# Optimization experiments

Measured on AMD Instinct MI355X. Metric: run time of the kernel, lower is better.

Reference implementation:

```python
import jax, jax.numpy as jnp
import numpy as np

N_NODES = 50000
N_EDGES = 1600000
IN_FEATS = 256
OUT_FEATS = 128
NEG_SLOPE = 0.2


def setup_inputs() -> dict:
    key = jax.random.key(0)
    k1, k2, k3, k4, k5, k6 = jax.random.split(key, 6)
    gain = np.sqrt(2.0)  # calculate_gain('relu')
    w_std = gain * np.sqrt(2.0 / (IN_FEATS + OUT_FEATS))  # xavier normal
    a_std = gain * np.sqrt(2.0 / (1 + OUT_FEATS))
    return {
        "feat": jax.random.normal(k1, (N_NODES, IN_FEATS), dtype=jnp.float32),
        "W": jax.random.normal(k2, (OUT_FEATS, IN_FEATS), dtype=jnp.float32) * w_std,
        "attn_l": jax.random.normal(k3, (1, OUT_FEATS), dtype=jnp.float32) * a_std,
        "attn_r": jax.random.normal(k4, (1, OUT_FEATS), dtype=jnp.float32) * a_std,
        "src": jax.random.randint(k5, (N_EDGES,), 0, N_NODES, dtype=jnp.int32),
        "dst": jax.random.randint(k6, (N_EDGES,), 0, N_NODES, dtype=jnp.int32),
    }


def reference(feat, W, attn_l, attn_r, src, dst):
    # h = fc(feat): [N, D]
    h = jnp.einsum("ni,di->nd", feat, W)
    # per-node attention logits
    el = jnp.sum(h * attn_l, axis=-1)  # [N]
    er = jnp.sum(h * attn_r, axis=-1)  # [N]
    # apply_edge: e_uv = el[u] + er[v], then leaky relu
    e = jax.nn.leaky_relu(el[src] + er[dst], NEG_SLOPE)  # [E]
    # edge softmax over incoming edges of each destination node
    m = jax.ops.segment_max(e, dst, num_segments=N_NODES)  # [N]
    m = jnp.where(jnp.isneginf(m), 0.0, m)  # nodes with no in-edges
    ex = jnp.exp(e - m[dst])  # [E]
    denom = jax.ops.segment_sum(ex, dst, num_segments=N_NODES)  # [N]
    alpha = ex / jnp.maximum(denom[dst], 1e-9)  # [E]
    # gspmv: rst[v] = sum_{(u->v)} alpha_uv * h[u]
    rst = jax.ops.segment_sum(h[src] * alpha[:, None], dst, num_segments=N_NODES)
    return rst
```

## Files before the change

kernel.cpp:

```cpp
#include <hip/hip_runtime.h>
#include <hip/hip_bf16.h>


#define IN_FEATS 256
#define OUT_FEATS 128
#define NBINS 256
#define CAPB_LOG 14
#define CAPB (1 << CAPB_LOG)
#define SCAT_BLOCKS 512
#define BIN_STRIDE 16

typedef __bf16 bf16x8 __attribute__((ext_vector_type(8)));
typedef float f32x4 __attribute__((ext_vector_type(4)));

__global__ void prep(const float* __restrict__ W, __bf16* __restrict__ Wb, int nw,
                     int* __restrict__ cur) {
    int i = blockIdx.x * 256 + threadIdx.x;
    if (i < nw) Wb[i] = (__bf16)W[i];
    if (i < NBINS) cur[i * BIN_STRIDE] = i << CAPB_LOG;
}

__global__ __launch_bounds__(256) void gemm_scatter(
    const float* __restrict__ feat, const __bf16* __restrict__ Wb,
    const float* __restrict__ attn_l, const float* __restrict__ attn_r,
    __bf16* __restrict__ hb, float* __restrict__ el, float* __restrict__ er,
    const int* __restrict__ src, const int* __restrict__ dst,
    int* __restrict__ bin_cur, unsigned* __restrict__ arena,
    int n, int E, int S) {
    __shared__ int h[NBINS];
    __shared__ int base[NBINS];

    if (blockIdx.x < S) {
        const int blk = blockIdx.x;
        const int t = threadIdx.x;
        h[t] = 0;
        __syncthreads();
        const int chunk = (E + SCAT_BLOCKS - 1) / SCAT_BLOCKS;
        const int beg = blk * chunk;
        const int end = min(beg + chunk, E);
        for (int i = beg + t; i < end; i += 256)
            atomicAdd(&h[dst[i] >> 8], 1);
        __syncthreads();
        if (h[t] > 0)
            base[t] = atomicAdd(&bin_cur[t * BIN_STRIDE], h[t]);
        h[t] = 0;
        __syncthreads();
        for (int i = beg + t; i < end; i += 256) {
            int d = dst[i];
            int bin = d >> 8;
            int pos = base[bin] + atomicAdd(&h[bin], 1);
            pos = min(pos, ((bin + 1) << CAPB_LOG) - 1);
            arena[pos] = ((unsigned)d << 16) | (unsigned)src[i];
        }
        return;
    }

    const int wid = threadIdx.x >> 6;
    const int lane = threadIdx.x & 63;
    const int s = lane & 15;
    const int q = lane >> 4;
    const int m0 = (blockIdx.x - S) * 64 + wid * 16;
    if (m0 >= n) return;

    const int mrow = min(m0 + s, n - 1);
    const float* arow = feat + (size_t)mrow * IN_FEATS + q * 8;

    f32x4 acc[8];
#pragma unroll
    for (int nt = 0; nt < 8; nt++) acc[nt] = (f32x4){0.f, 0.f, 0.f, 0.f};

#pragma unroll
    for (int ks = 0; ks < 8; ks++) {
        const int k0 = ks * 32;
        float4 f0 = *(const float4*)(arow + k0);
        float4 f1 = *(const float4*)(arow + k0 + 4);
        bf16x8 a;
        a[0] = (__bf16)f0.x; a[1] = (__bf16)f0.y; a[2] = (__bf16)f0.z; a[3] = (__bf16)f0.w;
        a[4] = (__bf16)f1.x; a[5] = (__bf16)f1.y; a[6] = (__bf16)f1.z; a[7] = (__bf16)f1.w;
#pragma unroll
        for (int nt = 0; nt < 8; nt++) {
            bf16x8 b = *(const bf16x8*)(Wb + (size_t)(nt * 16 + s) * IN_FEATS + k0 + q * 8);
            acc[nt] = __builtin_amdgcn_mfma_f32_16x16x32_bf16(a, b, acc[nt], 0, 0, 0);
        }
    }

    float al[8], ar[8];
#pragma unroll
    for (int nt = 0; nt < 8; nt++) {
        al[nt] = attn_l[nt * 16 + s];
        ar[nt] = attn_r[nt * 16 + s];
    }

#pragma unroll
    for (int r = 0; r < 4; r++) {
        const int row = m0 + q * 4 + r;
        const bool ok = row < n;
        float pl = 0.f, pr = 0.f;
#pragma unroll
        for (int nt = 0; nt < 8; nt++) {
            float v = acc[nt][r];
            if (ok) hb[(size_t)row * OUT_FEATS + nt * 16 + s] = (__bf16)v;
            pl += v * al[nt];
            pr += v * ar[nt];
        }
#pragma unroll
        for (int m = 1; m < 16; m <<= 1) {
            pl += __shfl_xor(pl, m);
            pr += __shfl_xor(pr, m);
        }
        if (ok && s == 0) {
            el[row] = pl;
            er[row] = pr;
        }
    }
}

__global__ __launch_bounds__(512) void build_csr(const unsigned* __restrict__ arena,
                                                 const int* __restrict__ bin_cur,
                                                 const float* __restrict__ el,
                                                 const float* __restrict__ er,
                                                 unsigned* __restrict__ edges,
                                                 int* __restrict__ row_beg,
                                                 int* __restrict__ row_end,
                                                 int N, int edges_cap) {
    __shared__ unsigned lds[CAPB];
    __shared__ int cnt[256];
    __shared__ int off[256];
    const int b = blockIdx.x;
    const int t = threadIdx.x;
    const int abeg = b << CAPB_LOG;
    const int cnt_in = min(bin_cur[b * BIN_STRIDE] - abeg, CAPB);

    for (int i = t; i < cnt_in; i += 512) lds[i] = arena[abeg + i];
    if (t < 256) cnt[t] = 0;
    __syncthreads();

    for (int i = t; i < cnt_in; i += 512)
        atomicAdd(&cnt[(lds[i] >> 16) & 255], 1);
    __syncthreads();
    if (t < 256) off[t] = cnt[t];
    __syncthreads();
    for (int o = 1; o < 256; o <<= 1) {
        int v = (t < 256 && t >= o) ? off[t - o] : 0;
        __syncthreads();
        if (t < 256) off[t] += v;
        __syncthreads();
    }
    int mycnt = 0, excl = 0;
    if (t < 256) {
        mycnt = cnt[t];
        excl = off[t] - mycnt;
    }
    __syncthreads();
    if (t < 256) {
        off[t] = excl;
        int v = (b << 8) + t;
        if (v < N) {
            row_beg[v] = abeg + excl;
            row_end[v] = abeg + excl + mycnt;
        }
        cnt[t] = 0;
    }
    __syncthreads();

    for (int i = t; i < cnt_in; i += 512) {
        unsigned e = lds[i];
        int d8 = (e >> 16) & 255;
        int u = (int)(e & 0xFFFFu);
        float x = el[u] + er[(b << 8) + d8];
        x = (x > 0.f) ? x : 0.2f * x;
        float w = __expf(x);
        int r = atomicAdd(&cnt[d8], 1);
        int pos = abeg + off[d8] + r;
        pos = min(pos, edges_cap - 1);
        edges[pos] = (__float_as_uint(w) & 0xFFFF0000u) | (unsigned)u;
    }
}

__global__ __launch_bounds__(256) void gat_kernel(const __bf16* __restrict__ hb,
                                                  const unsigned* __restrict__ edges,
                                                  const int* __restrict__ row_beg,
                                                  const int* __restrict__ row_end,
                                                  float* __restrict__ out, int n) {
    const int v = blockIdx.x * 4 + (threadIdx.x >> 6);
    if (v >= n) return;
    const int lane = threadIdx.x & 63;
    const int beg = row_beg[v];
    const int end = row_end[v];
    const unsigned* hbu = (const unsigned*)hb;

    float acc0 = 0.f, acc1 = 0.f, wsum = 0.f;
    for (int c0 = beg; c0 < end; c0 += 64) {
        const int nn = min(64, end - c0);
        int my = (c0 + lane < end) ? (int)edges[c0 + lane] : 0;

        int k = 0;
        for (; k + 8 <= nn; k += 8) {
#pragma unroll
            for (int tt = 0; tt < 8; tt++) {
                unsigned e = (unsigned)__shfl(my, k + tt);
                int u = (int)(e & 0xFFFFu);
                float w = __uint_as_float(e & 0xFFFF0000u);
                wsum += w;
                unsigned pair = hbu[(size_t)u * (OUT_FEATS / 2) + lane];
                acc0 += w * __uint_as_float(pair << 16);
                acc1 += w * __uint_as_float(pair & 0xffff0000u);
            }
        }
        for (; k < nn; k++) {
            unsigned e = (unsigned)__shfl(my, k);
            int u = (int)(e & 0xFFFFu);
            float w = __uint_as_float(e & 0xFFFF0000u);
            wsum += w;
            unsigned pair = hbu[(size_t)u * (OUT_FEATS / 2) + lane];
            acc0 += w * __uint_as_float(pair << 16);
            acc1 += w * __uint_as_float(pair & 0xffff0000u);
        }
    }
    const float dnm = fmaxf(wsum, 1e-9f);
    float2 o = make_float2(acc0 / dnm, acc1 / dnm);
    *(float2*)(out + (size_t)v * OUT_FEATS + lane * 2) = o;
}

extern "C" void kernel_launch(void* const* d_in, const int* in_sizes, int n_in,
                              void* d_out, int out_size, void* d_ws, size_t ws_size,
                              hipStream_t stream) {
    const float* feat   = (const float*)d_in[0];
    const float* W      = (const float*)d_in[1];
    const float* attn_l = (const float*)d_in[2];
    const float* attn_r = (const float*)d_in[3];
    const int*   src    = (const int*)d_in[4];
    const int*   dst    = (const int*)d_in[5];
    const int N = in_sizes[0] / IN_FEATS;
    const int E = in_sizes[4];
    float* out = (float*)d_out;

    char* p = (char*)d_ws;
    auto alloc = [&](size_t bytes) -> char* {
        char* r = p;
        p += (bytes + 255) & ~(size_t)255;
        return r;
    };
    const int nbuckets = (N + 255) / 256;
    const int edges_cap = nbuckets * CAPB;

    __bf16* hb    = (__bf16*)alloc((size_t)N * OUT_FEATS * sizeof(__bf16));
    __bf16* Wb    = (__bf16*)alloc((size_t)OUT_FEATS * IN_FEATS * sizeof(__bf16));
    float* el     = (float*)alloc((size_t)N * sizeof(float));
    float* er     = (float*)alloc((size_t)N * sizeof(float));
    int*   bin_cur = (int*)alloc((size_t)NBINS * BIN_STRIDE * sizeof(int));
    int*   row_beg = (int*)alloc((size_t)N * sizeof(int));
    int*   row_end = (int*)alloc((size_t)N * sizeof(int));
    unsigned* arena = (unsigned*)alloc((size_t)NBINS * CAPB * sizeof(unsigned));
    unsigned* edges = (unsigned*)alloc((size_t)edges_cap * sizeof(unsigned));

    prep<<<dim3((OUT_FEATS * IN_FEATS + 255) / 256), dim3(256), 0, stream>>>(
        W, Wb, OUT_FEATS * IN_FEATS, bin_cur);

    const int G = (N + 63) / 64;
    gemm_scatter<<<dim3(SCAT_BLOCKS + G), dim3(256), 0, stream>>>(
        feat, Wb, attn_l, attn_r, hb, el, er, src, dst, bin_cur, arena, N, E,
        SCAT_BLOCKS);

    build_csr<<<dim3(nbuckets), dim3(512), 0, stream>>>(arena, bin_cur, el, er, edges,
                                                        row_beg, row_end, N, edges_cap);

    gat_kernel<<<dim3((N + 3) / 4), dim3(256), 0, stream>>>(hb, edges, row_beg,
                                                            row_end, out, N);
}
```

Measured before the change: 219.6 us.

## Split scatter from GEMM and locally sort edges in LDS before global writes

Edge binning moves out of the fused GEMM kernel into its own kernel. That kernel counting-sorts each chunk of edges by bin in shared memory, so the writes to the global arena come out contiguous per bin instead of scattered. build_csr now reads the arena straight from global memory and stages the finished CSR records in LDS, then writes them out coalesced. The cost is an extra kernel launch and the loss of overlap between the GEMM and scatter work. The edges write no longer has a capacity clamp.

Result: slower. 226.2 us (+3.0%).

```diff
diff --git a/kernel.cpp b/kernel.cpp
--- a/kernel.cpp
+++ b/kernel.cpp
@@ -7,7 +7,7 @@
 #define NBINS 256
 #define CAPB_LOG 14
 #define CAPB (1 << CAPB_LOG)
-#define SCAT_BLOCKS 512
+#define SORT_CAP 4096
 #define BIN_STRIDE 16
 
 typedef __bf16 bf16x8 __attribute__((ext_vector_type(8)));
@@ -20,46 +20,16 @@
     if (i < NBINS) cur[i * BIN_STRIDE] = i << CAPB_LOG;
 }
 
-__global__ __launch_bounds__(256) void gemm_scatter(
+__global__ __launch_bounds__(256) void gemm(
     const float* __restrict__ feat, const __bf16* __restrict__ Wb,
     const float* __restrict__ attn_l, const float* __restrict__ attn_r,
     __bf16* __restrict__ hb, float* __restrict__ el, float* __restrict__ er,
-    const int* __restrict__ src, const int* __restrict__ dst,
-    int* __restrict__ bin_cur, unsigned* __restrict__ arena,
-    int n, int E, int S) {
-    __shared__ int h[NBINS];
-    __shared__ int base[NBINS];
-
-    if (blockIdx.x < S) {
-        const int blk = blockIdx.x;
-        const int t = threadIdx.x;
-        h[t] = 0;
-        __syncthreads();
-        const int chunk = (E + SCAT_BLOCKS - 1) / SCAT_BLOCKS;
-        const int beg = blk * chunk;
-        const int end = min(beg + chunk, E);
-        for (int i = beg + t; i < end; i += 256)
-            atomicAdd(&h[dst[i] >> 8], 1);
-        __syncthreads();
-        if (h[t] > 0)
-            base[t] = atomicAdd(&bin_cur[t * BIN_STRIDE], h[t]);
-        h[t] = 0;
-        __syncthreads();
-        for (int i = beg + t; i < end; i += 256) {
-            int d = dst[i];
-            int bin = d >> 8;
-            int pos = base[bin] + atomicAdd(&h[bin], 1);
-            pos = min(pos, ((bin + 1) << CAPB_LOG) - 1);
-            arena[pos] = ((unsigned)d << 16) | (unsigned)src[i];
-        }
-        return;
-    }
-
+    int n) {
     const int wid = threadIdx.x >> 6;
     const int lane = threadIdx.x & 63;
     const int s = lane & 15;
     const int q = lane >> 4;
-    const int m0 = (blockIdx.x - S) * 64 + wid * 16;
+    const int m0 = blockIdx.x * 64 + wid * 16;
     if (m0 >= n) return;
 
     const int mrow = min(m0 + s, n - 1);
@@ -115,6 +85,59 @@
     }
 }
 
+__global__ __launch_bounds__(256) void scatter(
+    const int* __restrict__ src, const int* __restrict__ dst,
+    int* __restrict__ bin_cur, unsigned* __restrict__ arena, int E, int nblk) {
+    __shared__ unsigned sorted[SORT_CAP];
+    __shared__ int h[NBINS];
+    __shared__ int off[NBINS];
+    __shared__ int gbase[NBINS];
+    const int t = threadIdx.x;
+    const int chunk = (E + nblk - 1) / nblk;
+    const int beg = blockIdx.x * chunk;
+    const int end = min(beg + chunk, E);
+
+    h[t] = 0;
+    __syncthreads();
+    for (int i = beg + t; i < end; i += 256)
+        atomicAdd(&h[dst[i] >> 8], 1);
+    __syncthreads();
+
+    off[t] = h[t];
+    __syncthreads();
+    for (int o = 1; o < 256; o <<= 1) {
+        int v = (t >= o) ? off[t - o] : 0;
+        __syncthreads();
+        off[t] += v;
+        __syncthreads();
+    }
+    const int mycnt = h[t];
+    const int excl = off[t] - mycnt;
+    __syncthreads();
+    off[t] = excl;
+    if (mycnt > 0)
+        gbase[t] = atomicAdd(&bin_cur[t * BIN_STRIDE], mycnt);
+    h[t] = 0;
+    __syncthreads();
+
+    for (int i = beg + t; i < end; i += 256) {
+        int d = dst[i];
+        int bin = d >> 8;
+        int r = atomicAdd(&h[bin], 1);
+        sorted[off[bin] + r] = ((unsigned)d << 16) | (unsigned)src[i];
+    }
+    __syncthreads();
+
+    const int tot = end - beg;
+    for (int j = t; j < tot; j += 256) {
+        unsigned w = sorted[j];
+        int bin = w >> 24;
+        int pos = gbase[bin] + (j - off[bin]);
+        pos = min(pos, ((bin + 1) << CAPB_LOG) - 1);
+        arena[pos] = w;
+    }
+}
+
 __global__ __launch_bounds__(512) void build_csr(const unsigned* __restrict__ arena,
                                                  const int* __restrict__ bin_cur,
                                                  const float* __restrict__ el,
@@ -122,7 +145,7 @@
                                                  unsigned* __restrict__ edges,
                                                  int* __restrict__ row_beg,
                                                  int* __restrict__ row_end,
-                                                 int N, int edges_cap) {
+                                                 int N) {
     __shared__ unsigned lds[CAPB];
     __shared__ int cnt[256];
     __shared__ int off[256];
@@ -131,12 +154,11 @@
     const int abeg = b << CAPB_LOG;
     const int cnt_in = min(bin_cur[b * BIN_STRIDE] - abeg, CAPB);
 
-    for (int i = t; i < cnt_in; i += 512) lds[i] = arena[abeg + i];
     if (t < 256) cnt[t] = 0;
     __syncthreads();
 
     for (int i = t; i < cnt_in; i += 512)
-        atomicAdd(&cnt[(lds[i] >> 16) & 255], 1);
+        atomicAdd(&cnt[(arena[abeg + i] >> 16) & 255], 1);
     __syncthreads();
     if (t < 256) off[t] = cnt[t];
     __syncthreads();
@@ -164,17 +186,19 @@
     __syncthreads();
 
     for (int i = t; i < cnt_in; i += 512) {
-        unsigned e = lds[i];
+        unsigned e = arena[abeg + i];
         int d8 = (e >> 16) & 255;
         int u = (int)(e & 0xFFFFu);
         float x = el[u] + er[(b << 8) + d8];
         x = (x > 0.f) ? x : 0.2f * x;
         float w = __expf(x);
         int r = atomicAdd(&cnt[d8], 1);
-        int pos = abeg + off[d8] + r;
-        pos = min(pos, edges_cap - 1);
-        edges[pos] = (__float_as_uint(w) & 0xFFFF0000u) | (unsigned)u;
-    }
+        lds[off[d8] + r] = (__float_as_uint(w) & 0xFFFF0000u) | (unsigned)u;
+    }
+    __syncthreads();
+
+    for (int i = t; i < cnt_in; i += 512)
+        edges[abeg + i] = lds[i];
 }
 
 __global__ __launch_bounds__(256) void gat_kernel(const __bf16* __restrict__ hb,
@@ -258,12 +282,13 @@
         W, Wb, OUT_FEATS * IN_FEATS, bin_cur);
 
     const int G = (N + 63) / 64;
-    gemm_scatter<<<dim3(SCAT_BLOCKS + G), dim3(256), 0, stream>>>(
-        feat, Wb, attn_l, attn_r, hb, el, er, src, dst, bin_cur, arena, N, E,
-        SCAT_BLOCKS);
+    gemm<<<dim3(G), dim3(256), 0, stream>>>(feat, Wb, attn_l, attn_r, hb, el, er, N);
+
+    const int nblk = max(512, (E + SORT_CAP - 1) / SORT_CAP);
+    scatter<<<dim3(nblk), dim3(256), 0, stream>>>(src, dst, bin_cur, arena, E, nblk);
 
     build_csr<<<dim3(nbuckets), dim3(512), 0, stream>>>(arena, bin_cur, el, er, edges,
-                                                        row_beg, row_end, N, edges_cap);
+                                                        row_beg, row_end, N);
 
     gat_kernel<<<dim3((N + 3) / 4), dim3(256), 0, stream>>>(hb, edges, row_beg,
                                                             row_end, out, N);
```
